# Kernel optimization log

Measured on AMD Instinct MI355X. Metric: run time of the kernel, lower is better.

## Reference

```python
import jax, jax.numpy as jnp
import numpy as np

B, S, E, H, F = 8, 1024, 1024, 16, 4096
D = E // H  # head_dim = 64
EPS = 1e-5


def setup_inputs() -> dict:
    key = jax.random.key(0)
    ks = jax.random.split(key, 12)
    s = 0.02
    return {
        "x": jax.random.normal(ks[0], (B, S, E), dtype=jnp.float32),
        # per-head projections (shared across heads), torch stores [out,in]; we use [in,out]
        "Wq": jax.random.normal(ks[1], (D, D), dtype=jnp.float32) * s,
        "Wk": jax.random.normal(ks[2], (D, D), dtype=jnp.float32) * s,
        "Wv": jax.random.normal(ks[3], (D, D), dtype=jnp.float32) * s,
        "Wo": jax.random.normal(ks[4], (E, E), dtype=jnp.float32) * s,
        "bo": jnp.zeros((E,), dtype=jnp.float32),
        "W1": jax.random.normal(ks[5], (E, F), dtype=jnp.float32) * s,
        "b1": jnp.zeros((F,), dtype=jnp.float32),
        "W2": jax.random.normal(ks[6], (F, E), dtype=jnp.float32) * s,
        "b2": jnp.zeros((E,), dtype=jnp.float32),
        "g1": jnp.ones((E,), dtype=jnp.float32),
        "beta1": jnp.zeros((E,), dtype=jnp.float32),
        "g2": jnp.ones((E,), dtype=jnp.float32),
        "beta2": jnp.zeros((E,), dtype=jnp.float32),
    }


def _layer_norm(x, g, b):
    m = jnp.mean(x, axis=-1, keepdims=True)
    v = jnp.mean(jnp.square(x - m), axis=-1, keepdims=True)
    return (x - m) * jax.lax.rsqrt(v + EPS) * g + b


def reference(x, Wq, Wk, Wv, Wo, bo, W1, b1, W2, b2, g1, beta1, g2, beta2):
    b, s, e = x.shape
    # --- attention sublayer (pre-norm) ---
    nx = _layer_norm(x, g1, beta1)
    h = nx.reshape(b, s, H, D)              # [B,S,H,D]
    q = h @ Wq                               # per-head linear, weight shared over heads
    k = h @ Wk
    v = h @ Wv
    energy = jnp.einsum('bqhd,bkhd->bhqk', q, k)  # full [B,H,S,S] scores
    mask = jnp.tril(jnp.ones((s, s), dtype=bool))
    energy = jnp.where(mask, energy, -jnp.inf)
    att = jax.nn.softmax(energy / jnp.sqrt(jnp.float32(e)), axis=-1)  # NOTE: scale by sqrt(embed_dim)
    o = jnp.einsum('bhqk,bkhd->bqhd', att, v).reshape(b, s, e)
    x = x + (o @ Wo + bo)
    # --- MLP sublayer (pre-norm); dropout is identity in eval ---
    nx = _layer_norm(x, g2, beta2)
    x = x + (jax.nn.relu(nx @ W1 + b1) @ W2 + b2)
    return x
```

## Files before the change

kernel.cpp:

```cpp
#include <hip/hip_runtime.h>

typedef unsigned short u16;
typedef __attribute__((ext_vector_type(4))) float f4;
typedef __attribute__((ext_vector_type(8))) short s8v;
typedef __attribute__((ext_vector_type(4))) unsigned short u16x4;

#define DEVINL __device__ __forceinline__

DEVINL float b2f(u16 u) { union { unsigned i; float f; } x; x.i = ((unsigned)u) << 16; return x.f; }
DEVINL u16 f2b(float f) {
  union { float f; unsigned i; } x; x.f = f;
  unsigned r = 0x7FFFu + ((x.i >> 16) & 1u);
  return (u16)((x.i + r) >> 16);
}

#define GLD_LDS16(g, l)                                                        \
  __builtin_amdgcn_global_load_lds((__attribute__((address_space(1))) void*)(g), \
                                   (__attribute__((address_space(3))) void*)(l), 16, 0, 0)

__global__ __launch_bounds__(256) void k_transpose(const float* __restrict__ in,
                                                   u16* __restrict__ out, int R, int C) {
  __shared__ float t[32][33];
  int tx = threadIdx.x & 31, ty = threadIdx.x >> 5;
  int c0 = blockIdx.x * 32, r0 = blockIdx.y * 32;
#pragma unroll
  for (int i = 0; i < 32; i += 8)
    t[ty + i][tx] = in[(long)(r0 + ty + i) * C + (c0 + tx)];
  __syncthreads();
#pragma unroll
  for (int i = 0; i < 32; i += 8)
    out[(long)(c0 + ty + i) * R + (r0 + tx)] = f2b(t[tx][ty + i]);
}

__global__ __launch_bounds__(256) void k_vtrans(const u16* __restrict__ v, u16* __restrict__ vt) {
  __shared__ u16 t[64][72];
  int bh = blockIdx.x, b = bh >> 4, h = bh & 15;
  int s0 = blockIdx.y * 64;
  int tid = threadIdx.x;
#pragma unroll
  for (int p = 0; p < 2; ++p) {
    int idx = p * 256 + tid;
    int sl = idx >> 3, c8 = (idx & 7) * 8;
    *(s8v*)(&t[sl][c8]) = *(const s8v*)(v + (((long)(b * 1024 + s0 + sl) * 16 + h) * 64) + c8);
  }
  __syncthreads();
#pragma unroll
  for (int p = 0; p < 2; ++p) {
    int idx = p * 256 + tid;
    int d = idx >> 3, c8 = (idx & 7) * 8;
    s8v o;
#pragma unroll
    for (int e = 0; e < 8; ++e) o[e] = (short)t[c8 + e][d];
    *(s8v*)(vt + ((long)bh * 64 + d) * 1024 + s0 + c8) = o;
  }
}

__global__ __launch_bounds__(256) void k_layernorm(const float* __restrict__ x,
                                                   const float* __restrict__ g,
                                                   const float* __restrict__ be,
                                                   u16* __restrict__ out) {
  long row = blockIdx.x;
  int tid = threadIdx.x;
  f4 v = ((const f4*)(x + row * 1024))[tid];
  float s = v[0] + v[1] + v[2] + v[3];
  float s2 = v[0] * v[0] + v[1] * v[1] + v[2] * v[2] + v[3] * v[3];
#pragma unroll
  for (int off = 32; off > 0; off >>= 1) {
    s += __shfl_down(s, off, 64);
    s2 += __shfl_down(s2, off, 64);
  }
  __shared__ float red[8];
  int wv = tid >> 6, ln = tid & 63;
  if (ln == 0) { red[wv] = s; red[4 + wv] = s2; }
  __syncthreads();
  s = red[0] + red[1] + red[2] + red[3];
  s2 = red[4] + red[5] + red[6] + red[7];
  float mean = s * (1.0f / 1024.0f);
  float var = s2 * (1.0f / 1024.0f) - mean * mean;
  float rs = rsqrtf(var + 1e-5f);
  f4 gg = ((const f4*)g)[tid];
  f4 bb = ((const f4*)be)[tid];
  u16x4 o;
#pragma unroll
  for (int i = 0; i < 4; ++i) o[i] = f2b((v[i] - mean) * rs * gg[i] + bb[i]);
  ((u16x4*)(out + row * 1024))[tid] = o;
}

__global__ __launch_bounds__(256) void k_qkv(const u16* __restrict__ nx, const u16* __restrict__ WqT,
                                             const u16* __restrict__ WkT, const u16* __restrict__ WvT,
                                             u16* __restrict__ q, u16* __restrict__ k,
                                             u16* __restrict__ v) {
  int tid = threadIdx.x, lane = tid & 63, wave = tid >> 6;
  int quad = lane >> 4, l16 = lane & 15;
  long rbase = (long)blockIdx.x * 64 + wave * 16;
  s8v a0 = *(const s8v*)(nx + (rbase + l16) * 64 + quad * 8);
  s8v a1 = *(const s8v*)(nx + (rbase + l16) * 64 + 32 + quad * 8);
  const u16* Ws[3] = {WqT, WkT, WvT};
  u16* Os[3] = {q, k, v};
#pragma unroll
  for (int t = 0; t < 3; ++t) {
#pragma unroll
    for (int j = 0; j < 4; ++j) {
      s8v b0 = *(const s8v*)(Ws[t] + (j * 16 + l16) * 64 + quad * 8);
      s8v b1 = *(const s8v*)(Ws[t] + (j * 16 + l16) * 64 + 32 + quad * 8);
      f4 acc = {0.f, 0.f, 0.f, 0.f};
      acc = __builtin_amdgcn_mfma_f32_16x16x32_bf16(a0, b0, acc, 0, 0, 0);
      acc = __builtin_amdgcn_mfma_f32_16x16x32_bf16(a1, b1, acc, 0, 0, 0);
#pragma unroll
      for (int r = 0; r < 4; ++r)
        Os[t][(rbase + quad * 4 + r) * 64 + j * 16 + l16] = f2b(acc[r]);
    }
  }
}

__global__ __launch_bounds__(256) void k_attn_mfma(const u16* __restrict__ q,
                                                   const u16* __restrict__ kk,
                                                   const u16* __restrict__ vt,
                                                   u16* __restrict__ o) {
  constexpr int LDK = 72;
  __shared__ u16 Ks[64 * LDK];
  __shared__ u16 Vt[64 * LDK];
  __shared__ u16 Ps[4][16 * LDK];
  int tid = threadIdx.x, lane = tid & 63, wave = tid >> 6;
  int quad = lane >> 4, l16 = lane & 15;
  int b = blockIdx.x >> 4, h = blockIdx.x & 15;
  int qi = (int)gridDim.y - 1 - (int)blockIdx.y;
  int q0 = qi * 64 + wave * 16;

  const u16* qp = q + (((long)(b * 1024 + q0 + l16)) * 16 + h) * 64;
  s8v aq0 = *(const s8v*)(qp + quad * 8);
  s8v aq1 = *(const s8v*)(qp + 32 + quad * 8);

  f4 O[4];
  float m_[4], l_[4];
#pragma unroll
  for (int jd = 0; jd < 4; ++jd) O[jd] = f4{0.f, 0.f, 0.f, 0.f};
#pragma unroll
  for (int r = 0; r < 4; ++r) { m_[r] = -__builtin_inff(); l_[r] = 0.f; }

  for (int kt = 0; kt <= qi; ++kt) {
    __syncthreads();
#pragma unroll
    for (int p = 0; p < 2; ++p) {
      int idx = p * 256 + tid;
      int row = idx >> 3, c8 = (idx & 7) * 8;
      *(s8v*)(Ks + row * LDK + c8) =
          *(const s8v*)(kk + (((long)(b * 1024 + kt * 64 + row)) * 16 + h) * 64 + c8);
      *(s8v*)(Vt + row * LDK + c8) =
          *(const s8v*)(vt + ((long)blockIdx.x * 64 + row) * 1024 + kt * 64 + c8);
    }
    __syncthreads();

    f4 sf[4];
#pragma unroll
    for (int jn = 0; jn < 4; ++jn) {
      s8v b0 = *(const s8v*)(Ks + (jn * 16 + l16) * LDK + quad * 8);
      s8v b1 = *(const s8v*)(Ks + (jn * 16 + l16) * LDK + 32 + quad * 8);
      f4 acc = f4{0.f, 0.f, 0.f, 0.f};
      acc = __builtin_amdgcn_mfma_f32_16x16x32_bf16(aq0, b0, acc, 0, 0, 0);
      acc = __builtin_amdgcn_mfma_f32_16x16x32_bf16(aq1, b1, acc, 0, 0, 0);
      sf[jn] = acc;
    }
    bool diag = (kt == qi);
    float rm[4];
#pragma unroll
    for (int r = 0; r < 4; ++r) rm[r] = -__builtin_inff();
#pragma unroll
    for (int jn = 0; jn < 4; ++jn)
#pragma unroll
      for (int r = 0; r < 4; ++r) {
        float v = sf[jn][r] * 0.03125f;
        if (diag && (jn * 16 + l16 > wave * 16 + quad * 4 + r)) v = -__builtin_inff();
        sf[jn][r] = v;
        rm[r] = fmaxf(rm[r], v);
      }
#pragma unroll
    for (int off = 1; off < 16; off <<= 1)
#pragma unroll
      for (int r = 0; r < 4; ++r) rm[r] = fmaxf(rm[r], __shfl_xor(rm[r], off, 64));
    float alpha[4], rs[4];
#pragma unroll
    for (int r = 0; r < 4; ++r) {
      float mn = fmaxf(m_[r], rm[r]);
      alpha[r] = __expf(m_[r] - mn);
      m_[r] = mn;
      rs[r] = 0.f;
    }
#pragma unroll
    for (int jn = 0; jn < 4; ++jn)
#pragma unroll
      for (int r = 0; r < 4; ++r) {
        float p = __expf(sf[jn][r] - m_[r]);
        rs[r] += p;
        Ps[wave][(quad * 4 + r) * LDK + jn * 16 + l16] = f2b(p);
      }
#pragma unroll
    for (int off = 1; off < 16; off <<= 1)
#pragma unroll
      for (int r = 0; r < 4; ++r) rs[r] += __shfl_xor(rs[r], off, 64);
#pragma unroll
    for (int r = 0; r < 4; ++r) l_[r] = l_[r] * alpha[r] + rs[r];
#pragma unroll
    for (int jd = 0; jd < 4; ++jd)
#pragma unroll
      for (int r = 0; r < 4; ++r) O[jd][r] *= alpha[r];
    asm volatile("s_waitcnt lgkmcnt(0)" ::: "memory");
    s8v p0 = *(const s8v*)(&Ps[wave][l16 * LDK + quad * 8]);
    s8v p1 = *(const s8v*)(&Ps[wave][l16 * LDK + 32 + quad * 8]);
#pragma unroll
    for (int jd = 0; jd < 4; ++jd) {
      s8v b0 = *(const s8v*)(Vt + (jd * 16 + l16) * LDK + quad * 8);
      s8v b1 = *(const s8v*)(Vt + (jd * 16 + l16) * LDK + 32 + quad * 8);
      O[jd] = __builtin_amdgcn_mfma_f32_16x16x32_bf16(p0, b0, O[jd], 0, 0, 0);
      O[jd] = __builtin_amdgcn_mfma_f32_16x16x32_bf16(p1, b1, O[jd], 0, 0, 0);
    }
  }
#pragma unroll
  for (int r = 0; r < 4; ++r) {
    float inv = 1.0f / l_[r];
    u16* op = o + (((long)(b * 1024 + q0 + quad * 4 + r)) * 16 + h) * 64;
#pragma unroll
    for (int jd = 0; jd < 4; ++jd) op[jd * 16 + l16] = f2b(O[jd][r] * inv);
  }
}

template <int EPI>
__global__ __launch_bounds__(256) void k_gemm_bt(const u16* __restrict__ A, const u16* __restrict__ BT,
                                                 const float* __restrict__ bias,
                                                 const float* __restrict__ resid,
                                                 void* __restrict__ outp, int M, int N, int K) {
  __shared__ u16 sA[3][128 * 32];
  __shared__ u16 sB[3][128 * 32];
  int tid = threadIdx.x, lane = tid & 63, wave = tid >> 6;
  int quad = lane >> 4, l16 = lane & 15;
  int wm = wave >> 1, wn = wave & 1;
  long bm = blockIdx.x, bn = blockIdx.y;
  int srow = tid >> 2, scol = (tid & 3) * 8;
  const u16* ga = A + (bm * 128 + srow) * (long)K + scol;
  const u16* gb = BT + (bn * 128 + srow) * (long)K + scol;
  int woff = wave * 1024;

  f4 acc[4][4];
#pragma unroll
  for (int i = 0; i < 4; ++i)
#pragma unroll
    for (int j = 0; j < 4; ++j) acc[i][j] = f4{0.f, 0.f, 0.f, 0.f};

#pragma unroll
  for (int t = 0; t < 2; ++t) {
    char* lA = (char*)&sA[t][0] + woff;
    char* lB = (char*)&sB[t][0] + woff;
    GLD_LDS16(ga + t * 32, lA);
    GLD_LDS16(ga + 64 * (long)K + t * 32, lA + 4096);
    GLD_LDS16(gb + t * 32, lB);
    GLD_LDS16(gb + 64 * (long)K + t * 32, lB + 4096);
  }

  int cur = 0;
  for (int k0 = 0; k0 < K; k0 += 32) {
    int k2 = k0 + 64;
    if (k2 < K) {
      asm volatile("s_waitcnt vmcnt(4)\n\ts_barrier" ::: "memory");
      int nb = cur >= 1 ? cur - 1 : 2;
      char* lA = (char*)&sA[nb][0] + woff;
      char* lB = (char*)&sB[nb][0] + woff;
      GLD_LDS16(ga + k2, lA);
      GLD_LDS16(ga + 64 * (long)K + k2, lA + 4096);
      GLD_LDS16(gb + k2, lB);
      GLD_LDS16(gb + 64 * (long)K + k2, lB + 4096);
    } else {
      asm volatile("s_waitcnt vmcnt(0)\n\ts_barrier" ::: "memory");
    }
    const u16* cA = sA[cur];
    const u16* cB = sB[cur];
    s8v aF[4], bF[4];
#pragma unroll
    for (int i = 0; i < 4; ++i)
      aF[i] = *(const s8v*)(cA + (wm * 64 + i * 16 + l16) * 32 + quad * 8);
#pragma unroll
    for (int j = 0; j < 4; ++j)
      bF[j] = *(const s8v*)(cB + (wn * 64 + j * 16 + l16) * 32 + quad * 8);
#pragma unroll
    for (int i = 0; i < 4; ++i)
#pragma unroll
      for (int j = 0; j < 4; ++j)
        acc[i][j] = __builtin_amdgcn_mfma_f32_16x16x32_bf16(aF[i], bF[j], acc[i][j], 0, 0, 0);
    cur = cur < 2 ? cur + 1 : 0;
  }

#pragma unroll
  for (int i = 0; i < 4; ++i) {
#pragma unroll
    for (int j = 0; j < 4; ++j) {
      long row = bm * 128 + wm * 64 + i * 16 + quad * 4;
      int col = (int)bn * 128 + wn * 64 + j * 16 + l16;
      float bcol = bias[col];
#pragma unroll
      for (int r = 0; r < 4; ++r) {
        float val = acc[i][j][r] + bcol;
        if (EPI == 1) {
          ((u16*)outp)[(row + r) * (long)N + col] = f2b(val > 0.f ? val : 0.f);
        } else {
          ((float*)outp)[(row + r) * (long)N + col] = resid[(row + r) * (long)N + col] + val;
        }
      }
    }
  }
}

template <int EPI>
__global__ __launch_bounds__(512) void k_gemm256(const u16* __restrict__ A,
                                                 const u16* __restrict__ BT,
                                                 const float* __restrict__ bias,
                                                 const float* __restrict__ resid,
                                                 void* __restrict__ outp, int M, int N, int K,
                                                 int lda) {
  __shared__ __align__(16) u16 S[65536];
  int tid = threadIdx.x, lane = tid & 63, wave = tid >> 6;
  int l16 = lane & 15, quad = lane >> 4;
  int wm = wave >> 2, wn = wave & 3;
  long bm = blockIdx.x, bn = blockIdx.y;
  int z = blockIdx.z;

  int rl = l16 & 7;
  int c0 = 8 * (quad ^ rl);
  int c1 = 8 * ((quad ^ 4) ^ rl);
  int rowA = (wm * 64 + l16) * 64;
  int rowB = (wn * 32 + l16) * 64;

  int Lb = tid * 16;
  int Ls = Lb ^ (((Lb >> 7) & 7) << 4);
  int r_ = Ls >> 7, kin = (Ls & 127) >> 1;
  const u16* pA = A + (bm * 256 + r_) * (long)lda + kin + (long)z * K;
  const u16* pB = BT + (bn * 256 + r_) * (long)lda + kin + (long)z * K;

  f4 acc[4][4][2];
#pragma unroll
  for (int q = 0; q < 4; ++q)
#pragma unroll
    for (int mi = 0; mi < 4; ++mi)
#pragma unroll
      for (int nj = 0; nj < 2; ++nj) acc[q][mi][nj] = f4{0.f, 0.f, 0.f, 0.f};
  s8v aF[4][2], bF[2][2][2];

#define BAR asm volatile("s_barrier" ::: "memory")
#define LGK0 asm volatile("s_waitcnt lgkmcnt(0)" ::: "memory")
#define WVM4 asm volatile("s_waitcnt vmcnt(4)" ::: "memory")
#define WVM0 asm volatile("s_waitcnt vmcnt(0)" ::: "memory")

#define STAGE(mat, half, t, buf)                                               \
  do {                                                                         \
    const u16* g_ = ((mat) ? pB : pA) + (long)(half) * 128 * lda + (t) * 64;   \
    char* l_ = ((char*)S) + ((buf) * 32768 + (mat) * 16384 + (half) * 8192) * 2 + wave * 1024; \
    GLD_LDS16(g_, l_);                                                         \
    GLD_LDS16(g_ + 64 * (long)lda, l_ + 8192);                                 \
  } while (0)

#define LDA(buf, mh)                                                           \
  do {                                                                         \
    const u16* p_ = S + (buf) * 32768 + (mh) * 8192 + rowA;                    \
    _Pragma("unroll") for (int mi = 0; mi < 4; ++mi) {                         \
      aF[mi][0] = *(const s8v*)(p_ + mi * 1024 + c0);                          \
      aF[mi][1] = *(const s8v*)(p_ + mi * 1024 + c1);                          \
    }                                                                          \
  } while (0)

#define LDB(buf, nh, set)                                                      \
  do {                                                                         \
    const u16* p_ = S + (buf) * 32768 + 16384 + (nh) * 8192 + rowB;            \
    _Pragma("unroll") for (int nj = 0; nj < 2; ++nj) {                         \
      bF[set][nj][0] = *(const s8v*)(p_ + nj * 1024 + c0);                     \
      bF[set][nj][1] = *(const s8v*)(p_ + nj * 1024 + c1);                     \
    }                                                                          \
  } while (0)

#define MM(q)                                                                  \
  do {                                                                         \
    _Pragma("unroll") for (int mi = 0; mi < 4; ++mi)                           \
        _Pragma("unroll") for (int nj = 0; nj < 2; ++nj) {                     \
      acc[q][mi][nj] = __builtin_amdgcn_mfma_f32_16x16x32_bf16(                \
          aF[mi][0], bF[(q) & 1][nj][0], acc[q][mi][nj], 0, 0, 0);             \
      acc[q][mi][nj] = __builtin_amdgcn_mfma_f32_16x16x32_bf16(                \
          aF[mi][1], bF[(q) & 1][nj][1], acc[q][mi][nj], 0, 0, 0);             \
    }                                                                          \
  } while (0)

#define PHASES(t, LAST)                                                        \
                                             \
  LDA(0, 0); LDB(0, 0, 0); STAGE(0, 1, (t) + 1, 1);                            \
  BAR; LGK0; __builtin_amdgcn_s_setprio(1); MM(0); __builtin_amdgcn_s_setprio(0); BAR; \
                                                           \
  LDB(0, 1, 1); STAGE(1, 1, (t) + 1, 1);                                       \
  BAR; LGK0; __builtin_amdgcn_s_setprio(1); MM(1); __builtin_amdgcn_s_setprio(0); BAR; \
                                                           \
  LDA(0, 1); if (!(LAST)) STAGE(0, 0, (t) + 2, 0);                             \
  BAR; LGK0; __builtin_amdgcn_s_setprio(1); MM(2); __builtin_amdgcn_s_setprio(0); BAR; \
                                          \
  if (!(LAST)) STAGE(1, 0, (t) + 2, 0);                                        \
  __builtin_amdgcn_s_setprio(1); MM(3); __builtin_amdgcn_s_setprio(0);         \
  if (LAST) { WVM0; } else { WVM4; }                                           \
  BAR;                                                                         \
                                           \
  LDA(1, 0); LDB(1, 0, 0); if (!(LAST)) STAGE(0, 1, (t) + 2, 0);               \
  BAR; LGK0; __builtin_amdgcn_s_setprio(1); MM(0); __builtin_amdgcn_s_setprio(0); BAR; \
                                                           \
  LDB(1, 1, 1); if (!(LAST)) STAGE(1, 1, (t) + 2, 0);                          \
  BAR; LGK0; __builtin_amdgcn_s_setprio(1); MM(1); __builtin_amdgcn_s_setprio(0); BAR; \
                                                           \
  LDA(1, 1); if (!(LAST)) STAGE(0, 0, (t) + 3, 1);                             \
  BAR; LGK0; __builtin_amdgcn_s_setprio(1); MM(2); __builtin_amdgcn_s_setprio(0); BAR; \
                                                           \
  if (!(LAST)) STAGE(1, 0, (t) + 3, 1);                                        \
  __builtin_amdgcn_s_setprio(1); MM(3); __builtin_amdgcn_s_setprio(0);         \
  if (!(LAST)) { WVM4; BAR; }

  STAGE(0, 0, 0, 0);
  STAGE(1, 0, 0, 0);
  STAGE(0, 1, 0, 0);
  STAGE(1, 1, 0, 0);
  STAGE(0, 0, 1, 1);
  STAGE(1, 0, 1, 1);
  WVM4; BAR;

  int NI = K >> 7;
  for (int i = 0; i < NI - 1; ++i) {
    int t = 2 * i;
    PHASES(t, 0);
  }
  {
    int t = 2 * (NI - 1);
    PHASES(t, 1);
  }

#undef PHASES
#undef MM
#undef LDB
#undef LDA
#undef STAGE
#undef WVM0
#undef WVM4
#undef LGK0
#undef BAR

  float* P0 = (EPI == 0) ? ((float*)outp + (long)z * M * N) : nullptr;
#pragma unroll
  for (int q = 0; q < 4; ++q) {
    int mh = q >> 1, nh = q & 1;
#pragma unroll
    for (int mi = 0; mi < 4; ++mi) {
#pragma unroll
      for (int nj = 0; nj < 2; ++nj) {
        long row = bm * 256 + mh * 128 + wm * 64 + mi * 16 + quad * 4;
        int col = (int)bn * 256 + nh * 128 + wn * 32 + nj * 16 + l16;
        float bcol = 0.f;
        if (EPI != 0) bcol = bias[col];
#pragma unroll
        for (int rr = 0; rr < 4; ++rr) {
          float val = acc[q][mi][nj][rr] + bcol;
          if (EPI == 0) {
            P0[(row + rr) * (long)N + col] = val;
          } else if (EPI == 1) {
            ((u16*)outp)[(row + rr) * (long)N + col] = f2b(val > 0.f ? val : 0.f);
          } else {
            ((float*)outp)[(row + rr) * (long)N + col] =
                resid[(row + rr) * (long)N + col] + val;
          }
        }
      }
    }
  }
}

__global__ __launch_bounds__(256) void k_combine(const float* __restrict__ P,
                                                 const float* __restrict__ resid,
                                                 const float* __restrict__ bias,
                                                 float* __restrict__ out) {
  const f4* P0 = (const f4*)P;
  const f4* P1 = P0 + 2097152;
  const f4* R = (const f4*)resid;
  const f4* Bv = (const f4*)bias;
  f4* O = (f4*)out;
  for (int i = blockIdx.x * 256 + threadIdx.x; i < 2097152; i += 2048 * 256) {
    f4 a = P0[i], b = P1[i], r = R[i], bb = Bv[i & 255];
    O[i] = a + b + r + bb;
  }
}

extern "C" void kernel_launch(void* const* d_in, const int* in_sizes, int n_in, void* d_out,
                              int out_size, void* d_ws, size_t ws_size, hipStream_t stream) {
  const float* x = (const float*)d_in[0];
  const float* Wq = (const float*)d_in[1];
  const float* Wk = (const float*)d_in[2];
  const float* Wv = (const float*)d_in[3];
  const float* Wo = (const float*)d_in[4];
  const float* bo = (const float*)d_in[5];
  const float* W1 = (const float*)d_in[6];
  const float* b1 = (const float*)d_in[7];
  const float* W2 = (const float*)d_in[8];
  const float* b2 = (const float*)d_in[9];
  const float* g1 = (const float*)d_in[10];
  const float* be1 = (const float*)d_in[11];
  const float* g2 = (const float*)d_in[12];
  const float* be2 = (const float*)d_in[13];

  char* ws = (char*)d_ws;
  const size_t MB = 1ull << 20;
  u16* nx = (u16*)(ws + 0);
  u16* qb = (u16*)(ws + 16 * MB);
  u16* kb = (u16*)(ws + 32 * MB);
  u16* vb = (u16*)(ws + 48 * MB);
  float* x1 = (float*)(ws + 64 * MB);
  u16* h1 = (u16*)(ws + 96 * MB);
  u16* vtr = (u16*)(ws + 96 * MB);
  u16* WoT = (u16*)(ws + 160 * MB);
  u16* W1T = (u16*)(ws + 162 * MB);
  u16* W2T = (u16*)(ws + 170 * MB);
  u16* WqT = (u16*)(ws + 178 * MB);
  u16* WkT = WqT + 64 * 64;
  u16* WvT = WkT + 64 * 64;
  u16* ob = nx;
  u16* nx2 = qb;
  float* Pk = (float*)ws;

  k_transpose<<<dim3(32, 32), 256, 0, stream>>>(Wo, WoT, 1024, 1024);
  k_transpose<<<dim3(128, 32), 256, 0, stream>>>(W1, W1T, 1024, 4096);
  k_transpose<<<dim3(32, 128), 256, 0, stream>>>(W2, W2T, 4096, 1024);
  k_transpose<<<dim3(2, 2), 256, 0, stream>>>(Wq, WqT, 64, 64);
  k_transpose<<<dim3(2, 2), 256, 0, stream>>>(Wk, WkT, 64, 64);
  k_transpose<<<dim3(2, 2), 256, 0, stream>>>(Wv, WvT, 64, 64);

  k_layernorm<<<8192, 256, 0, stream>>>(x, g1, be1, nx);
  k_qkv<<<2048, 256, 0, stream>>>(nx, WqT, WkT, WvT, qb, kb, vb);
  k_vtrans<<<dim3(128, 16), 256, 0, stream>>>(vb, vtr);
  k_attn_mfma<<<dim3(128, 16), 256, 0, stream>>>(qb, kb, vtr, ob);
  k_gemm_bt<2><<<dim3(64, 8), 256, 0, stream>>>(ob, WoT, bo, x, x1, 8192, 1024, 1024);

  k_layernorm<<<8192, 256, 0, stream>>>(x1, g2, be2, nx2);
  k_gemm256<1><<<dim3(32, 16, 1), 512, 0, stream>>>(nx2, W1T, b1, nullptr, h1, 8192, 4096, 1024, 1024);
  k_gemm256<0><<<dim3(32, 4, 2), 512, 0, stream>>>(h1, W2T, nullptr, nullptr, Pk, 8192, 1024, 2048, 4096);
  k_combine<<<2048, 256, 0, stream>>>(Pk, x1, b2, (float*)d_out);
}
```

Baseline: 439.7 us.

## Add 256x128-tile pipelined GEMM for Wo and W2, drop split-K and combine

Introduces a 512-thread GEMM kernel with a 256x128 output tile, XOR-swizzled LDS, double-buffered direct global-to-LDS staging and a fused bias+residual epilogue. It replaces the simpler 128x128 Wo projection GEMM. It also replaces the split-K W2 GEMM and its separate combine kernel, removing the fp32 partial-sum round trip through memory. The tradeoff is that the W2 GEMM now launches only 256 blocks doing the full K=4096, which lowers parallelism on a large-CU part compared with the split-K version.

```diff
diff --git a/kernel.cpp b/kernel.cpp
--- a/kernel.cpp
+++ b/kernel.cpp
@@ -225,90 +225,6 @@
 }
 
 template <int EPI>
-__global__ __launch_bounds__(256) void k_gemm_bt(const u16* __restrict__ A, const u16* __restrict__ BT,
-                                                 const float* __restrict__ bias,
-                                                 const float* __restrict__ resid,
-                                                 void* __restrict__ outp, int M, int N, int K) {
-  __shared__ u16 sA[3][128 * 32];
-  __shared__ u16 sB[3][128 * 32];
-  int tid = threadIdx.x, lane = tid & 63, wave = tid >> 6;
-  int quad = lane >> 4, l16 = lane & 15;
-  int wm = wave >> 1, wn = wave & 1;
-  long bm = blockIdx.x, bn = blockIdx.y;
-  int srow = tid >> 2, scol = (tid & 3) * 8;
-  const u16* ga = A + (bm * 128 + srow) * (long)K + scol;
-  const u16* gb = BT + (bn * 128 + srow) * (long)K + scol;
-  int woff = wave * 1024;
-
-  f4 acc[4][4];
-#pragma unroll
-  for (int i = 0; i < 4; ++i)
-#pragma unroll
-    for (int j = 0; j < 4; ++j) acc[i][j] = f4{0.f, 0.f, 0.f, 0.f};
-
-#pragma unroll
-  for (int t = 0; t < 2; ++t) {
-    char* lA = (char*)&sA[t][0] + woff;
-    char* lB = (char*)&sB[t][0] + woff;
-    GLD_LDS16(ga + t * 32, lA);
-    GLD_LDS16(ga + 64 * (long)K + t * 32, lA + 4096);
-    GLD_LDS16(gb + t * 32, lB);
-    GLD_LDS16(gb + 64 * (long)K + t * 32, lB + 4096);
-  }
-
-  int cur = 0;
-  for (int k0 = 0; k0 < K; k0 += 32) {
-    int k2 = k0 + 64;
-    if (k2 < K) {
-      asm volatile("s_waitcnt vmcnt(4)\n\ts_barrier" ::: "memory");
-      int nb = cur >= 1 ? cur - 1 : 2;
-      char* lA = (char*)&sA[nb][0] + woff;
-      char* lB = (char*)&sB[nb][0] + woff;
-      GLD_LDS16(ga + k2, lA);
-      GLD_LDS16(ga + 64 * (long)K + k2, lA + 4096);
-      GLD_LDS16(gb + k2, lB);
-      GLD_LDS16(gb + 64 * (long)K + k2, lB + 4096);
-    } else {
-      asm volatile("s_waitcnt vmcnt(0)\n\ts_barrier" ::: "memory");
-    }
-    const u16* cA = sA[cur];
-    const u16* cB = sB[cur];
-    s8v aF[4], bF[4];
-#pragma unroll
-    for (int i = 0; i < 4; ++i)
-      aF[i] = *(const s8v*)(cA + (wm * 64 + i * 16 + l16) * 32 + quad * 8);
-#pragma unroll
-    for (int j = 0; j < 4; ++j)
-      bF[j] = *(const s8v*)(cB + (wn * 64 + j * 16 + l16) * 32 + quad * 8);
-#pragma unroll
-    for (int i = 0; i < 4; ++i)
-#pragma unroll
-      for (int j = 0; j < 4; ++j)
-        acc[i][j] = __builtin_amdgcn_mfma_f32_16x16x32_bf16(aF[i], bF[j], acc[i][j], 0, 0, 0);
-    cur = cur < 2 ? cur + 1 : 0;
-  }
-
-#pragma unroll
-  for (int i = 0; i < 4; ++i) {
-#pragma unroll
-    for (int j = 0; j < 4; ++j) {
-      long row = bm * 128 + wm * 64 + i * 16 + quad * 4;
-      int col = (int)bn * 128 + wn * 64 + j * 16 + l16;
-      float bcol = bias[col];
-#pragma unroll
-      for (int r = 0; r < 4; ++r) {
-        float val = acc[i][j][r] + bcol;
-        if (EPI == 1) {
-          ((u16*)outp)[(row + r) * (long)N + col] = f2b(val > 0.f ? val : 0.f);
-        } else {
-          ((float*)outp)[(row + r) * (long)N + col] = resid[(row + r) * (long)N + col] + val;
-        }
-      }
-    }
-  }
-}
-
-template <int EPI>
 __global__ __launch_bounds__(512) void k_gemm256(const u16* __restrict__ A,
                                                  const u16* __restrict__ BT,
                                                  const float* __restrict__ bias,
@@ -386,30 +302,22 @@
   } while (0)
 
 #define PHASES(t, LAST)                                                        \
-                                             \
   LDA(0, 0); LDB(0, 0, 0); STAGE(0, 1, (t) + 1, 1);                            \
   BAR; LGK0; __builtin_amdgcn_s_setprio(1); MM(0); __builtin_amdgcn_s_setprio(0); BAR; \
-                                                           \
   LDB(0, 1, 1); STAGE(1, 1, (t) + 1, 1);                                       \
   BAR; LGK0; __builtin_amdgcn_s_setprio(1); MM(1); __builtin_amdgcn_s_setprio(0); BAR; \
-                                                           \
   LDA(0, 1); if (!(LAST)) STAGE(0, 0, (t) + 2, 0);                             \
   BAR; LGK0; __builtin_amdgcn_s_setprio(1); MM(2); __builtin_amdgcn_s_setprio(0); BAR; \
-                                          \
   if (!(LAST)) STAGE(1, 0, (t) + 2, 0);                                        \
   __builtin_amdgcn_s_setprio(1); MM(3); __builtin_amdgcn_s_setprio(0);         \
   if (LAST) { WVM0; } else { WVM4; }                                           \
   BAR;                                                                         \
-                                           \
   LDA(1, 0); LDB(1, 0, 0); if (!(LAST)) STAGE(0, 1, (t) + 2, 0);               \
   BAR; LGK0; __builtin_amdgcn_s_setprio(1); MM(0); __builtin_amdgcn_s_setprio(0); BAR; \
-                                                           \
   LDB(1, 1, 1); if (!(LAST)) STAGE(1, 1, (t) + 2, 0);                          \
   BAR; LGK0; __builtin_amdgcn_s_setprio(1); MM(1); __builtin_amdgcn_s_setprio(0); BAR; \
-                                                           \
   LDA(1, 1); if (!(LAST)) STAGE(0, 0, (t) + 3, 1);                             \
   BAR; LGK0; __builtin_amdgcn_s_setprio(1); MM(2); __builtin_amdgcn_s_setprio(0); BAR; \
-                                                           \
   if (!(LAST)) STAGE(1, 0, (t) + 3, 1);                                        \
   __builtin_amdgcn_s_setprio(1); MM(3); __builtin_amdgcn_s_setprio(0);         \
   if (!(LAST)) { WVM4; BAR; }
@@ -471,18 +379,146 @@
   }
 }
 
-__global__ __launch_bounds__(256) void k_combine(const float* __restrict__ P,
-                                                 const float* __restrict__ resid,
-                                                 const float* __restrict__ bias,
-                                                 float* __restrict__ out) {
-  const f4* P0 = (const f4*)P;
-  const f4* P1 = P0 + 2097152;
-  const f4* R = (const f4*)resid;
-  const f4* Bv = (const f4*)bias;
-  f4* O = (f4*)out;
-  for (int i = blockIdx.x * 256 + threadIdx.x; i < 2097152; i += 2048 * 256) {
-    f4 a = P0[i], b = P1[i], r = R[i], bb = Bv[i & 255];
-    O[i] = a + b + r + bb;
+__global__ __launch_bounds__(512) void k_gemm256n128(const u16* __restrict__ A,
+                                                     const u16* __restrict__ BT,
+                                                     const float* __restrict__ bias,
+                                                     const float* __restrict__ resid,
+                                                     float* __restrict__ outp,
+                                                     int M, int N, int K, int lda) {
+  __shared__ __align__(16) u16 S[49152];
+  int tid = threadIdx.x, lane = tid & 63, wave = tid >> 6;
+  int l16 = lane & 15, quad = lane >> 4;
+  int wm = wave >> 1, wn = wave & 1;
+  long bm = blockIdx.x, bn = blockIdx.y;
+
+  int rl = l16 & 7;
+  int c0 = 8 * (quad ^ rl);
+  int c1 = 8 * ((quad ^ 4) ^ rl);
+  int rowA = (wm >> 1) * 8192 + ((wm & 1) * 64 + l16) * 64;
+  int rowB = 16384 + (wn * 64 + l16) * 64;
+
+  int Lb = tid * 16;
+  int Ls = Lb ^ (((Lb >> 7) & 7) << 4);
+  int r_ = Ls >> 7, kin = (Ls & 127) >> 1;
+  const u16* pA = A + (bm * 256 + r_) * (long)lda + kin;
+  const u16* pB = BT + (bn * 128 + r_) * (long)lda + kin;
+
+  f4 acc[4][4];
+#pragma unroll
+  for (int mi = 0; mi < 4; ++mi)
+#pragma unroll
+    for (int nj = 0; nj < 4; ++nj) acc[mi][nj] = f4{0.f, 0.f, 0.f, 0.f};
+  s8v aF[4][2], bF[2][2];
+
+#define BAR asm volatile("s_barrier" ::: "memory")
+#define LGK0 asm volatile("s_waitcnt lgkmcnt(0)" ::: "memory")
+#define WVM4 asm volatile("s_waitcnt vmcnt(4)" ::: "memory")
+#define WVM0 asm volatile("s_waitcnt vmcnt(0)" ::: "memory")
+
+#define STAGEA(t, buf)                                                         \
+  do {                                                                         \
+    const u16* g_ = pA + (t) * 64;                                             \
+    char* l_ = ((char*)S) + (buf) * 49152 + wave * 1024;                       \
+    GLD_LDS16(g_, l_);                                                         \
+    GLD_LDS16(g_ + 64 * (long)lda, l_ + 8192);                                 \
+    GLD_LDS16(g_ + 128 * (long)lda, l_ + 16384);                               \
+    GLD_LDS16(g_ + 192 * (long)lda, l_ + 24576);                               \
+  } while (0)
+
+#define STAGEB(t, buf)                                                         \
+  do {                                                                         \
+    const u16* g_ = pB + (t) * 64;                                             \
+    char* l_ = ((char*)S) + (buf) * 49152 + 32768 + wave * 1024;               \
+    GLD_LDS16(g_, l_);                                                         \
+    GLD_LDS16(g_ + 64 * (long)lda, l_ + 8192);                                 \
+  } while (0)
+
+#define LDAn(buf)                                                              \
+  do {                                                                         \
+    const u16* p_ = S + (buf) * 24576 + rowA;                                  \
+    _Pragma("unroll") for (int mi = 0; mi < 4; ++mi) {                         \
+      aF[mi][0] = *(const s8v*)(p_ + mi * 1024 + c0);                          \
+      aF[mi][1] = *(const s8v*)(p_ + mi * 1024 + c1);                          \
+    }                                                                          \
+  } while (0)
+
+#define LDBn(buf, nh)                                                          \
+  do {                                                                         \
+    const u16* p_ = S + (buf) * 24576 + rowB + (nh) * 2048;                    \
+    _Pragma("unroll") for (int nj2 = 0; nj2 < 2; ++nj2) {                      \
+      bF[nj2][0] = *(const s8v*)(p_ + nj2 * 1024 + c0);                        \
+      bF[nj2][1] = *(const s8v*)(p_ + nj2 * 1024 + c1);                        \
+    }                                                                          \
+  } while (0)
+
+#define MMn(nh)                                                                \
+  do {                                                                         \
+    _Pragma("unroll") for (int mi = 0; mi < 4; ++mi)                           \
+        _Pragma("unroll") for (int nj2 = 0; nj2 < 2; ++nj2) {                  \
+      acc[mi][(nh) * 2 + nj2] = __builtin_amdgcn_mfma_f32_16x16x32_bf16(       \
+          aF[mi][0], bF[nj2][0], acc[mi][(nh) * 2 + nj2], 0, 0, 0);            \
+      acc[mi][(nh) * 2 + nj2] = __builtin_amdgcn_mfma_f32_16x16x32_bf16(       \
+          aF[mi][1], bF[nj2][1], acc[mi][(nh) * 2 + nj2], 0, 0, 0);            \
+    }                                                                          \
+  } while (0)
+
+#define PHASES(t, LAST)                                                        \
+                                                                      \
+  LDAn(0); LDBn(0, 0); STAGEB((t) + 1, 1);                                     \
+  BAR; LGK0; __builtin_amdgcn_s_setprio(1); MMn(0); __builtin_amdgcn_s_setprio(0); BAR; \
+                                                                      \
+  LDBn(0, 1); if (!(LAST)) STAGEA((t) + 2, 0);                                 \
+  BAR; LGK0; __builtin_amdgcn_s_setprio(1); MMn(1); __builtin_amdgcn_s_setprio(0); \
+  if (LAST) { WVM0; } else { WVM4; }                                           \
+  BAR;                                                                         \
+                                                                      \
+  LDAn(1); LDBn(1, 0); if (!(LAST)) STAGEB((t) + 2, 0);                        \
+  BAR; LGK0; __builtin_amdgcn_s_setprio(1); MMn(0); __builtin_amdgcn_s_setprio(0); BAR; \
+                                                                      \
+  LDBn(1, 1); if (!(LAST)) STAGEA((t) + 3, 1);                                 \
+  BAR; LGK0; __builtin_amdgcn_s_setprio(1); MMn(1); __builtin_amdgcn_s_setprio(0); \
+  if (!(LAST)) { WVM4; }                                                       \
+  BAR;
+
+  STAGEA(0, 0);
+  STAGEB(0, 0);
+  STAGEA(1, 1);
+  WVM4; BAR;
+
+  int NI = K >> 7;
+  for (int i = 0; i < NI - 1; ++i) {
+    int t = 2 * i;
+    PHASES(t, 0);
+  }
+  {
+    int t = 2 * (NI - 1);
+    PHASES(t, 1);
+  }
+
+#undef PHASES
+#undef MMn
+#undef LDBn
+#undef LDAn
+#undef STAGEB
+#undef STAGEA
+#undef WVM0
+#undef WVM4
+#undef LGK0
+#undef BAR
+
+#pragma unroll
+  for (int mi = 0; mi < 4; ++mi) {
+#pragma unroll
+    for (int nj = 0; nj < 4; ++nj) {
+      long row = bm * 256 + wm * 64 + mi * 16 + quad * 4;
+      int col = (int)bn * 128 + wn * 64 + nj * 16 + l16;
+      float bcol = bias[col];
+#pragma unroll
+      for (int rr = 0; rr < 4; ++rr) {
+        outp[(row + rr) * (long)N + col] =
+            resid[(row + rr) * (long)N + col] + acc[mi][nj][rr] + bcol;
+      }
+    }
   }
 }
 
@@ -520,7 +556,6 @@
   u16* WvT = WkT + 64 * 64;
   u16* ob = nx;
   u16* nx2 = qb;
-  float* Pk = (float*)ws;
 
   k_transpose<<<dim3(32, 32), 256, 0, stream>>>(Wo, WoT, 1024, 1024);
   k_transpose<<<dim3(128, 32), 256, 0, stream>>>(W1, W1T, 1024, 4096);
@@ -533,10 +568,9 @@
   k_qkv<<<2048, 256, 0, stream>>>(nx, WqT, WkT, WvT, qb, kb, vb);
   k_vtrans<<<dim3(128, 16), 256, 0, stream>>>(vb, vtr);
   k_attn_mfma<<<dim3(128, 16), 256, 0, stream>>>(qb, kb, vtr, ob);
-  k_gemm_bt<2><<<dim3(64, 8), 256, 0, stream>>>(ob, WoT, bo, x, x1, 8192, 1024, 1024);
+  k_gemm256n128<<<dim3(32, 8), 512, 0, stream>>>(ob, WoT, bo, x, x1, 8192, 1024, 1024, 1024);
 
   k_layernorm<<<8192, 256, 0, stream>>>(x1, g2, be2, nx2);
   k_gemm256<1><<<dim3(32, 16, 1), 512, 0, stream>>>(nx2, W1T, b1, nullptr, h1, 8192, 4096, 1024, 1024);
-  k_gemm256<0><<<dim3(32, 4, 2), 512, 0, stream>>>(h1, W2T, nullptr, nullptr, Pk, 8192, 1024, 2048, 4096);
-  k_combine<<<2048, 256, 0, stream>>>(Pk, x1, b2, (float*)d_out);
-}
+  k_gemm256n128<<<dim3(32, 8), 512, 0, stream>>>(h1, W2T, b2, x1, (float*)d_out, 8192, 1024, 4096, 4096);
+}
```

Measured after the change: 414.9 us. 1.06x faster.
